# Kernel tuning notes

Hardware: AMD Instinct MI355X
Metric: run time of the kernel (lower is better)

## Reference

```python
import jax, jax.numpy as jnp
import numpy as np

C, B, N, L = 4, 8, 4096, 1024


def setup_inputs() -> dict:
    key = jax.random.key(0)
    inputs = jax.random.normal(key, (C, B, N, L), dtype=jnp.float32)
    return {"inputs": inputs}


def reference(inputs) -> jnp.ndarray:
    # Original: for each [N, L] box_input, divide each row elementwise by
    # range(1..L) and reduce_sum over the last axis. Vectorized across all
    # leading dims via broadcasting. Output shape [C, B, N].
    L_ = inputs.shape[-1]
    probability_numbers = jnp.arange(1, L_ + 1, dtype=inputs.dtype)  # [L]
    return jnp.sum(inputs / probability_numbers, axis=-1)
```

## Files before the change

kernel.cpp:

```cpp
#include <hip/hip_runtime.h>


constexpr int kL = 1024;
constexpr int kBlocks = 2048;
constexpr int kThreads = 256;

__global__ __launch_bounds__(kThreads) void FractalDimension_kernel(
    const float* __restrict__ in, float* __restrict__ out, int rows) {
  const int lane = threadIdx.x & 63;
  const int waveId = blockIdx.x * (kThreads >> 6) + (threadIdx.x >> 6);
  const int nWaves = kBlocks * (kThreads >> 6);

  float r[4][4];
#pragma unroll
  for (int k = 0; k < 4; ++k)
#pragma unroll
    for (int c = 0; c < 4; ++c)
      r[k][c] = 1.0f / (float)((lane + k * 64) * 4 + c + 1);

  const int trips = rows / nWaves;
#pragma unroll 2
  for (int i = 0; i < trips; ++i) {
    const int row = waveId + i * nWaves;
    const float4* p = reinterpret_cast<const float4*>(in + (size_t)row * kL);
    float4 v0 = p[lane];
    float4 v1 = p[lane + 64];
    float4 v2 = p[lane + 128];
    float4 v3 = p[lane + 192];

    float s = v0.x * r[0][0] + v0.y * r[0][1] + v0.z * r[0][2] + v0.w * r[0][3];
    s += v1.x * r[1][0] + v1.y * r[1][1] + v1.z * r[1][2] + v1.w * r[1][3];
    s += v2.x * r[2][0] + v2.y * r[2][1] + v2.z * r[2][2] + v2.w * r[2][3];
    s += v3.x * r[3][0] + v3.y * r[3][1] + v3.z * r[3][2] + v3.w * r[3][3];

#pragma unroll
    for (int off = 32; off > 0; off >>= 1)
      s += __shfl_down(s, off, 64);

    if (lane == 0) out[row] = s;
  }

  for (int row = trips * nWaves + waveId; row < rows; row += nWaves) {
    const float4* p = reinterpret_cast<const float4*>(in + (size_t)row * kL);
    float s = 0.f;
#pragma unroll
    for (int k = 0; k < 4; ++k) {
      float4 v = p[lane + k * 64];
      s += v.x * r[k][0] + v.y * r[k][1] + v.z * r[k][2] + v.w * r[k][3];
    }
#pragma unroll
    for (int off = 32; off > 0; off >>= 1)
      s += __shfl_down(s, off, 64);
    if (lane == 0) out[row] = s;
  }
}

extern "C" void kernel_launch(void* const* d_in, const int* in_sizes, int n_in,
                              void* d_out, int out_size, void* d_ws, size_t ws_size,
                              hipStream_t stream) {
  const float* in = (const float*)d_in[0];
  float* out = (float*)d_out;
  const int rows = in_sizes[0] / kL;
  FractalDimension_kernel<<<kBlocks, kThreads, 0, stream>>>(in, out, rows);
}
```

Measured before the change: 667.2 us.

## Process sixteen rows per wave with batched loads and deferred reductions

Replaces the grid-stride loop, which handled one row per wave per iteration, with a fixed mapping of sixteen contiguous rows per wave. Eight 16-byte loads are issued back to back before any arithmetic so more memory requests are in flight. The cross-lane reduction is done once at the end for all sixteen accumulators, and lanes 0-15 write the results together. In exchange, the kernel uses more registers and assumes the row count is a multiple of sixteen, with no tail handling for rows beyond a partial group.

```diff
diff --git a/kernel.cpp b/kernel.cpp
--- a/kernel.cpp
+++ b/kernel.cpp
@@ -2,57 +2,58 @@
 
 
 constexpr int kL = 1024;
-constexpr int kBlocks = 2048;
 constexpr int kThreads = 256;
+constexpr int kRowsPerWave = 16;
+
+typedef float f4 __attribute__((ext_vector_type(4)));
 
 __global__ __launch_bounds__(kThreads) void FractalDimension_kernel(
     const float* __restrict__ in, float* __restrict__ out, int rows) {
   const int lane = threadIdx.x & 63;
-  const int waveId = blockIdx.x * (kThreads >> 6) + (threadIdx.x >> 6);
-  const int nWaves = kBlocks * (kThreads >> 6);
+  const int wave = blockIdx.x * (kThreads >> 6) + (threadIdx.x >> 6);
+  const int rowBase = wave * kRowsPerWave;
+  if (rowBase >= rows) return;
 
   float r[4][4];
 #pragma unroll
   for (int k = 0; k < 4; ++k)
 #pragma unroll
     for (int c = 0; c < 4; ++c)
-      r[k][c] = 1.0f / (float)((lane + k * 64) * 4 + c + 1);
+      r[k][c] = 1.0f / (float)((k * 64 + lane) * 4 + c + 1);
 
-  const int trips = rows / nWaves;
-#pragma unroll 2
-  for (int i = 0; i < trips; ++i) {
-    const int row = waveId + i * nWaves;
-    const float4* p = reinterpret_cast<const float4*>(in + (size_t)row * kL);
-    float4 v0 = p[lane];
-    float4 v1 = p[lane + 64];
-    float4 v2 = p[lane + 128];
-    float4 v3 = p[lane + 192];
+  const f4* p = reinterpret_cast<const f4*>(in + (size_t)rowBase * kL);
 
-    float s = v0.x * r[0][0] + v0.y * r[0][1] + v0.z * r[0][2] + v0.w * r[0][3];
-    s += v1.x * r[1][0] + v1.y * r[1][1] + v1.z * r[1][2] + v1.w * r[1][3];
-    s += v2.x * r[2][0] + v2.y * r[2][1] + v2.z * r[2][2] + v2.w * r[2][3];
-    s += v3.x * r[3][0] + v3.y * r[3][1] + v3.z * r[3][2] + v3.w * r[3][3];
+  float acc[kRowsPerWave];
+#pragma unroll
+  for (int j = 0; j < kRowsPerWave; ++j) acc[j] = 0.0f;
 
 #pragma unroll
-    for (int off = 32; off > 0; off >>= 1)
-      s += __shfl_down(s, off, 64);
-
-    if (lane == 0) out[row] = s;
+  for (int k = 0; k < 4; ++k) {
+#pragma unroll
+    for (int jj = 0; jj < kRowsPerWave; jj += 8) {
+      f4 v[8];
+#pragma unroll
+      for (int j = 0; j < 8; ++j)
+        v[j] = p[(size_t)(jj + j) * 256 + k * 64 + lane];
+#pragma unroll
+      for (int j = 0; j < 8; ++j)
+        acc[jj + j] += v[j].x * r[k][0] + v[j].y * r[k][1] +
+                       v[j].z * r[k][2] + v[j].w * r[k][3];
+    }
   }
 
-  for (int row = trips * nWaves + waveId; row < rows; row += nWaves) {
-    const float4* p = reinterpret_cast<const float4*>(in + (size_t)row * kL);
-    float s = 0.f;
 #pragma unroll
-    for (int k = 0; k < 4; ++k) {
-      float4 v = p[lane + k * 64];
-      s += v.x * r[k][0] + v.y * r[k][1] + v.z * r[k][2] + v.w * r[k][3];
-    }
+  for (int off = 32; off > 0; off >>= 1) {
 #pragma unroll
-    for (int off = 32; off > 0; off >>= 1)
-      s += __shfl_down(s, off, 64);
-    if (lane == 0) out[row] = s;
+    for (int j = 0; j < kRowsPerWave; ++j)
+      acc[j] += __shfl_xor(acc[j], off, 64);
   }
+
+  float res = acc[0];
+#pragma unroll
+  for (int j = 1; j < kRowsPerWave; ++j)
+    res = (lane == j) ? acc[j] : res;
+  if (lane < kRowsPerWave) out[rowBase + lane] = res;
 }
 
 extern "C" void kernel_launch(void* const* d_in, const int* in_sizes, int n_in,
@@ -61,5 +62,7 @@
   const float* in = (const float*)d_in[0];
   float* out = (float*)d_out;
   const int rows = in_sizes[0] / kL;
-  FractalDimension_kernel<<<kBlocks, kThreads, 0, stream>>>(in, out, rows);
+  const int wavesNeeded = (rows + kRowsPerWave - 1) / kRowsPerWave;
+  const int blocks = (wavesNeeded + (kThreads >> 6) - 1) / (kThreads >> 6);
+  FractalDimension_kernel<<<blocks, kThreads, 0, stream>>>(in, out, rows);
 }
```

Result: no change. 672.2 us (+0.7%).
